# Optimization experiments

Measured on AMD Instinct MI355X. Metric: run time of the kernel, lower is better.

Reference implementation:

```python
import jax, jax.numpy as jnp
import numpy as np

B = 262144
N_DIM = 8
N_SPLIT = 4
DEPTH = 8
WIDTH = 32
ALPHA = 0.6
LOGSCALE_FACTOR = 3.0


def setup_inputs() -> dict:
    key = jax.random.key(0)
    ks = jax.random.split(key, 8)
    n_out = (N_DIM - N_SPLIT) * 2  # 8
    inp = {
        "x": jax.random.normal(ks[0], (B, N_DIM), dtype=jnp.float32),
        "logdet": jnp.zeros((B, 1), dtype=jnp.float32),
        # actnorm params (stacked over depth)
        "b": jnp.zeros((DEPTH, 1, N_DIM), dtype=jnp.float32),
        "logs": jnp.zeros((DEPTH, 1, N_DIM), dtype=jnp.float32),
        # affine coupling params
        "log_gamma": jnp.zeros((DEPTH, 1, N_DIM - N_SPLIT), dtype=jnp.float32),
        "W1": jax.random.normal(ks[1], (DEPTH, N_SPLIT, WIDTH), dtype=jnp.float32) / np.sqrt(N_SPLIT),
        "b1": jnp.zeros((DEPTH, WIDTH), dtype=jnp.float32),
        "W2": jax.random.normal(ks[2], (DEPTH, WIDTH, WIDTH), dtype=jnp.float32) / np.sqrt(WIDTH),
        "b2": jnp.zeros((DEPTH, WIDTH), dtype=jnp.float32),
        "Wf": jax.random.normal(ks[3], (DEPTH, WIDTH, n_out), dtype=jnp.float32) / np.sqrt(WIDTH),
        "bf": jnp.zeros((DEPTH, n_out), dtype=jnp.float32),
    }
    return inp


def _flow_forward(x, logdet, b, logs, log_gamma, W1, b1, W2, b2, Wf, bf):
    z = x
    ld = logdet
    for i in range(DEPTH):
        # ---- actnorm (with data-dependent init, detached as in torch) ----
        m = jnp.mean(z, axis=0, keepdims=True)
        v = jnp.mean(jnp.square(z - m), axis=0, keepdims=True)
        b_init = jax.lax.stop_gradient(-m)
        logs_init = jax.lax.stop_gradient(
            jnp.log(1.0 / (jnp.sqrt(v) + 1e-6)) / LOGSCALE_FACTOR)
        s = jnp.clip(logs[i] + logs_init, -5.0, 5.0)
        z = (z + (b[i] + b_init)) * jnp.exp(s)
        ld = ld + jnp.sum(s)
        # ---- affine coupling ----
        z1 = z[:, :N_SPLIT]
        z2 = z[:, N_SPLIT:]
        h = jax.nn.relu(z1 @ W1[i] + b1[i])
        h = jax.nn.relu(h @ W2[i] + b2[i])
        h = h @ Wf[i] + bf[i]                      # [B, 2*(n_dim-ns)]
        shift = h[:, 0::2]
        scale = ALPHA * jnp.tanh(h[:, 1::2])
        shift = jnp.exp(jnp.clip(log_gamma[i], -5.0, 5.0)) * jnp.tanh(shift)
        z2 = z2 + scale * z2 + shift
        ld = ld + jnp.sum(jnp.log1p(scale), axis=1, keepdims=True)
        z = jnp.concatenate([z1, z2], axis=1)
        # ---- flip ----
        z = z[:, ::-1]
    return z, ld


def reference(x, logdet, b, logs, log_gamma, W1, b1, W2, b2, Wf, bf):
    return _flow_forward(x, logdet, b, logs, log_gamma, W1, b1, W2, b2, Wf, bf)
```

## Files before the change

### kernel.cpp

```cpp
#include <hip/hip_runtime.h>

#define B_ROWS 262144
#define TPB 1024
#define NBLK 256
#define NSLOT 64
#define NGRP 16
#define PADW 32

#define SLOT_DW (16 * NSLOT * PADW)
#define SLOTS_TOTAL_DW (9 * SLOT_DW)

#define GC_OFF   32
#define GF_OFF   (32 + NGRP * PADW)
#define BAR_DWORDS (GF_OFF + NGRP * PADW)

#define ZERO_DWORDS (SLOTS_TOTAL_DW + BAR_DWORDS)

typedef _Float16 f16;
typedef __attribute__((ext_vector_type(2))) __fp16 fp16x2_t;
typedef __attribute__((ext_vector_type(8))) _Float16 f16x8;
typedef __attribute__((ext_vector_type(4))) float f32x4;
typedef __attribute__((ext_vector_type(16))) float f32x16;
typedef __attribute__((ext_vector_type(2))) unsigned u32x2;

__device__ __forceinline__ float fast_tanh(float x) {
    float e = __expf(2.0f * x);
    return 1.0f - 2.0f * __builtin_amdgcn_rcpf(e + 1.0f);
}
__device__ __forceinline__ float pkh(float a, float b) {
    fp16x2_t h = __builtin_amdgcn_cvt_pkrtz(a, b);
    return __builtin_bit_cast(float, h);
}
__device__ __forceinline__ f16x8 mk8(float a, float b, float c, float d) {
    f32x4 v = {a, b, c, d};
    return __builtin_bit_cast(f16x8, v);
}
__device__ __forceinline__ float bcf(unsigned u) { return __builtin_bit_cast(float, u); }
__device__ __forceinline__ u32x2 pls(float a, float b) {
    return __builtin_amdgcn_permlane32_swap(
        __builtin_bit_cast(unsigned, a), __builtin_bit_cast(unsigned, b),
        false, false);
}

__device__ __forceinline__ void gbar(unsigned* bar, unsigned target) {
    __syncthreads();
    if (threadIdx.x == 0) {
        const int g = blockIdx.x >> 4;
        unsigned old = __hip_atomic_fetch_add(bar + GC_OFF + g * PADW, 1u,
                                              __ATOMIC_ACQ_REL,
                                              __HIP_MEMORY_SCOPE_AGENT);
        if (old + 1 == target * (NBLK / NGRP)) {
            unsigned ro = __hip_atomic_fetch_add(bar, 1u, __ATOMIC_ACQ_REL,
                                                 __HIP_MEMORY_SCOPE_AGENT);
            if (ro + 1 == target * NGRP) {
                __threadfence();
                #pragma unroll
                for (int i = 0; i < NGRP; ++i)
                    __hip_atomic_store(bar + GF_OFF + i * PADW, target,
                                       __ATOMIC_RELAXED,
                                       __HIP_MEMORY_SCOPE_AGENT);
            }
        }
        unsigned* gf = bar + GF_OFF + g * PADW;
        while (__hip_atomic_load(gf, __ATOMIC_RELAXED,
                                 __HIP_MEMORY_SCOPE_AGENT) < target)
            __builtin_amdgcn_s_sleep(2);
        (void)__hip_atomic_load(gf, __ATOMIC_ACQUIRE, __HIP_MEMORY_SCOPE_AGENT);
    }
    __syncthreads();
}

#define PKBLK 80
__global__ void __launch_bounds__(256)
pack_weights(const float* __restrict__ W1, const float* __restrict__ W2,
             const float* __restrict__ Wf,
             f16* __restrict__ w1pk, f16* __restrict__ w2pk, f16* __restrict__ wfpk,
             float* __restrict__ zbase)
{
    int i = blockIdx.x * 256 + threadIdx.x;
    if (i < 16384) {
        int which = i >> 13;
        int t  = i & 8191;
        int j  = t & 7;
        int ln = (t >> 3) & 63;
        int kh = (t >> 9) & 1;
        int L  = t >> 10;
        int k  = kh * 16 + ((ln >> 5) << 3) + j;
        if (which == 0) {
            w2pk[t] = (f16)W2[L * 1024 + k * 32 + (ln & 31)];
        } else {
            int row = ln & 31;
            wfpk[t] = (row < 8) ? (f16)Wf[L * 256 + k * 8 + row] : (f16)0.f;
        }
    } else {
        int t  = i - 16384;
        int j  = t & 7;
        int ln = (t >> 3) & 63;
        int L  = t >> 9;
        int k  = ((ln >> 5) << 3) + j;
        w1pk[t] = (k < 4) ? (f16)W1[L * 128 + k * 32 + (ln & 31)] : (f16)0.f;
    }
    float4 zv = {0.f, 0.f, 0.f, 0.f};
    float4* zp = reinterpret_cast<float4*>(zbase);
    const int total4 = ZERO_DWORDS >> 2;
    for (int t4 = i; t4 < total4; t4 += PKBLK * 256)
        zp[t4] = zv;
}

__global__ void __launch_bounds__(TPB, 4)
flow_fused(const float* __restrict__ x,    const float* __restrict__ logdet,
           const float* __restrict__ bvec, const float* __restrict__ logs,
           const float* __restrict__ log_gamma,
           const float* __restrict__ b1,   const float* __restrict__ b2,
           const float* __restrict__ bf,
           const f16* __restrict__ w1pk,   const f16* __restrict__ w2pk,
           const f16* __restrict__ wfpk,
           float* __restrict__ out,        float* slots,
           unsigned* __restrict__ bar)
{
    const int tid  = threadIdx.x;
    const int bid  = blockIdx.x;
    const int lane = tid & 63;
    const int wid  = tid >> 6;
    const bool lo  = lane < 32;
    const int slot = bid & (NSLOT - 1);
    const int br = ((lane & 1) << 3) | ((lane & 2) << 1) | ((lane & 4) >> 1) | ((lane & 8) >> 3);
    const size_t r0 = (size_t)bid * TPB + tid;

    __shared__ float lred[16 * 16];

    float z[8];
    {
        const float4* p0 = reinterpret_cast<const float4*>(x + r0 * 8);
        float4 a = p0[0], c = p0[1];
        z[0]=a.x; z[1]=a.y; z[2]=a.z; z[3]=a.w;
        z[4]=c.x; z[5]=c.y; z[6]=c.z; z[7]=c.w;
    }
    float ldv = logdet[r0];

    {
        float acc[16];
        #pragma unroll
        for (int j = 0; j < 8; ++j) { acc[j] = z[j]; acc[8 + j] = z[j] * z[j]; }
        #pragma unroll
        for (int i = 0; i < 8; ++i) {
            float snd = (lane & 1) ? acc[i] : acc[8 + i];
            float kp  = (lane & 1) ? acc[8 + i] : acc[i];
            acc[i] = kp + __shfl_xor(snd, 1, 64);
        }
        #pragma unroll
        for (int i = 0; i < 4; ++i) {
            float snd = (lane & 2) ? acc[i] : acc[4 + i];
            float kp  = (lane & 2) ? acc[4 + i] : acc[i];
            acc[i] = kp + __shfl_xor(snd, 2, 64);
        }
        #pragma unroll
        for (int i = 0; i < 2; ++i) {
            float snd = (lane & 4) ? acc[i] : acc[2 + i];
            float kp  = (lane & 4) ? acc[2 + i] : acc[i];
            acc[i] = kp + __shfl_xor(snd, 4, 64);
        }
        {
            float snd = (lane & 8) ? acc[0] : acc[1];
            float kp  = (lane & 8) ? acc[1] : acc[0];
            acc[0] = kp + __shfl_xor(snd, 8, 64);
        }
        acc[0] += __shfl_xor(acc[0], 16, 64);
        acc[0] += __shfl_xor(acc[0], 32, 64);
        if (lane < 16) lred[wid * 16 + br] = acc[0];
        __syncthreads();
        if (tid < 16) {
            float s = 0.f;
            #pragma unroll
            for (int w = 0; w < 16; ++w) s += lred[w * 16 + tid];
            __hip_atomic_fetch_add(slots + (size_t)(tid * NSLOT + slot) * PADW, s,
                                   __ATOMIC_RELAXED, __HIP_MEMORY_SCOPE_AGENT);
        }
    }
    gbar(bar, 1);

    const f16x8* w1p = reinterpret_cast<const f16x8*>(w1pk);
    const f16x8* w2p = reinterpret_cast<const f16x8*>(w2pk);
    const f16x8* wfp = reinterpret_cast<const f16x8*>(wfpk);

    #pragma unroll 1
    for (int L = 0; L < 8; ++L) {
        const f16x8 W1A = w1p[L * 64 + lane];
        const f16x8 A0  = w2p[(L * 2 + 0) * 64 + lane];
        const f16x8 A1  = w2p[(L * 2 + 1) * 64 + lane];
        const f16x8 F0  = wfp[(L * 2 + 0) * 64 + lane];
        const f16x8 F1  = wfp[(L * 2 + 1) * 64 + lane];

        float es[8], beta[8], gfac[4], sum_s;
        {
            const float* sl = slots + (size_t)L * SLOT_DW;
            if (wid == 0) {
                float a16[16];
                #pragma unroll
                for (int j = 0; j < 16; ++j)
                    a16[j] = __hip_atomic_load(sl + (size_t)(j * NSLOT + lane) * PADW,
                                               __ATOMIC_RELAXED,
                                               __HIP_MEMORY_SCOPE_AGENT);
                #pragma unroll
                for (int d = 1; d < 64; d <<= 1) {
                    #pragma unroll
                    for (int j = 0; j < 16; ++j) a16[j] += __shfl_xor(a16[j], d, 64);
                }
                const float invB = 1.0f / (float)B_ROWS;
                float lv[21];
                float ss = 0.f;
                #pragma unroll
                for (int j = 0; j < 8; ++j) {
                    float m = a16[j] * invB;
                    float q = a16[8 + j] * invB;
                    float v = q - m * m;
                    v = v < 0.f ? 0.f : v;
                    float li = -(1.0f / 3.0f) * __logf(sqrtf(v) + 1e-6f);
                    float s = logs[L * 8 + j] + li;
                    s = s < -5.f ? -5.f : (s > 5.f ? 5.f : s);
                    lv[j]     = __expf(s);
                    lv[8 + j] = bvec[L * 8 + j] - m;
                    ss += s;
                }
                #pragma unroll
                for (int j = 0; j < 4; ++j) {
                    float lg = log_gamma[L * 4 + j];
                    lg = lg < -5.f ? -5.f : (lg > 5.f ? 5.f : lg);
                    lv[16 + j] = __expf(lg);
                }
                lv[20] = ss;
                if (lane == 0) {
                    #pragma unroll
                    for (int j = 0; j < 21; ++j) lred[j] = lv[j];
                }
            }
            __syncthreads();
            #pragma unroll
            for (int j = 0; j < 8; ++j) { es[j] = lred[j]; beta[j] = lred[8 + j]; }
            #pragma unroll
            for (int j = 0; j < 4; ++j) gfac[j] = lred[16 + j];
            sum_s = lred[20];
            __syncthreads();
        }

        #pragma unroll
        for (int j = 0; j < 8; ++j)
            z[j] = (z[j] + beta[j]) * es[j];

        const float* vb1 = b1 + L * 32;
        const float* vb2 = b2 + L * 32;
        const float* vbf = bf + L * 8;

        float zp0 = pkh(z[0], z[1]);
        float zp1 = pkh(z[2], z[3]);
        u32x2 s0 = pls(zp0, 0.f);
        u32x2 s1 = pls(zp1, 0.f);
        f16x8 Z0 = mk8(bcf(s0[0]), bcf(s1[0]), 0.f, 0.f);
        f16x8 Z1 = mk8(bcf(s0[1]), bcf(s1[1]), 0.f, 0.f);

        f32x16 g0 = {}, g1 = {};
        g0 = __builtin_amdgcn_mfma_f32_32x32x16_f16(W1A, Z0, g0, 0, 0, 0);
        g1 = __builtin_amdgcn_mfma_f32_32x32x16_f16(W1A, Z1, g1, 0, 0, 0);

        float qg0[8], qg1[8];
        {
            float h0[16], h1v[16];
            #pragma unroll
            for (int r = 0; r < 16; ++r) {
                int wlo = (r & 3) + 8 * (r >> 2);
                float bsel = lo ? vb1[wlo] : vb1[wlo + 4];
                float a = g0[r] + bsel; h0[r]  = a > 0.f ? a : 0.f;
                float b = g1[r] + bsel; h1v[r] = b > 0.f ? b : 0.f;
            }
            #pragma unroll
            for (int c = 0; c < 8; ++c) {
                qg0[c] = pkh(h0[2 * c], h0[2 * c + 1]);
                qg1[c] = pkh(h1v[2 * c], h1v[2 * c + 1]);
            }
        }

        u32x2 pA = pls(qg0[0], qg0[2]);
        u32x2 pB = pls(qg0[1], qg0[3]);
        u32x2 pC = pls(qg0[4], qg0[6]);
        u32x2 pD = pls(qg0[5], qg0[7]);
        f16x8 B00 = mk8(bcf(pA[0]), bcf(pB[0]), bcf(pA[1]), bcf(pB[1]));
        f16x8 B01 = mk8(bcf(pC[0]), bcf(pD[0]), bcf(pC[1]), bcf(pD[1]));
        pA = pls(qg1[0], qg1[2]);
        pB = pls(qg1[1], qg1[3]);
        pC = pls(qg1[4], qg1[6]);
        pD = pls(qg1[5], qg1[7]);
        f16x8 B10 = mk8(bcf(pA[0]), bcf(pB[0]), bcf(pA[1]), bcf(pB[1]));
        f16x8 B11 = mk8(bcf(pC[0]), bcf(pD[0]), bcf(pC[1]), bcf(pD[1]));

        f32x16 d0 = {}, d1 = {};
        d0 = __builtin_amdgcn_mfma_f32_32x32x16_f16(A0, B00, d0, 0, 0, 0);
        d0 = __builtin_amdgcn_mfma_f32_32x32x16_f16(A1, B01, d0, 0, 0, 0);
        d1 = __builtin_amdgcn_mfma_f32_32x32x16_f16(A0, B10, d1, 0, 0, 0);
        d1 = __builtin_amdgcn_mfma_f32_32x32x16_f16(A1, B11, d1, 0, 0, 0);

        float P0[8], P1[8];
        {
            float h2g0[16], h2g1[16];
            #pragma unroll
            for (int r = 0; r < 16; ++r) {
                int wlo = (r & 3) + 8 * (r >> 2);
                float bsel = lo ? vb2[wlo] : vb2[wlo + 4];
                float a = d0[r] + bsel; h2g0[r] = a > 0.f ? a : 0.f;
                float b = d1[r] + bsel; h2g1[r] = b > 0.f ? b : 0.f;
            }
            #pragma unroll
            for (int c = 0; c < 8; ++c) {
                P0[c] = pkh(h2g0[2 * c], h2g0[2 * c + 1]);
                P1[c] = pkh(h2g1[2 * c], h2g1[2 * c + 1]);
            }
        }

        u32x2 pE = pls(P0[0], P0[2]);
        u32x2 pF = pls(P0[1], P0[3]);
        u32x2 pG = pls(P0[4], P0[6]);
        u32x2 pH = pls(P0[5], P0[7]);
        f16x8 C00 = mk8(bcf(pE[0]), bcf(pF[0]), bcf(pE[1]), bcf(pF[1]));
        f16x8 C01 = mk8(bcf(pG[0]), bcf(pH[0]), bcf(pG[1]), bcf(pH[1]));
        pE = pls(P1[0], P1[2]);
        pF = pls(P1[1], P1[3]);
        pG = pls(P1[4], P1[6]);
        pH = pls(P1[5], P1[7]);
        f16x8 C10 = mk8(bcf(pE[0]), bcf(pF[0]), bcf(pE[1]), bcf(pF[1]));
        f16x8 C11 = mk8(bcf(pG[0]), bcf(pH[0]), bcf(pG[1]), bcf(pH[1]));

        f32x16 e0 = {}, e1 = {};
        e0 = __builtin_amdgcn_mfma_f32_32x32x16_f16(F0, C00, e0, 0, 0, 0);
        e0 = __builtin_amdgcn_mfma_f32_32x32x16_f16(F1, C01, e0, 0, 0, 0);
        e1 = __builtin_amdgcn_mfma_f32_32x32x16_f16(F0, C10, e1, 0, 0, 0);
        e1 = __builtin_amdgcn_mfma_f32_32x32x16_f16(F1, C11, e1, 0, 0, 0);

        float h3[8];
        #pragma unroll
        for (int r = 0; r < 4; ++r) {
            u32x2 pe = pls(e0[r], e1[r]);
            h3[r]     = bcf(pe[0]) + vbf[r];
            h3[r + 4] = bcf(pe[1]) + vbf[r + 4];
        }

        float nacc[16];
        {
            float ldl = 0.f;
            float nz[8];
            #pragma unroll
            for (int j = 0; j < 4; ++j) {
                float sc = 0.6f * fast_tanh(h3[2 * j + 1]);
                float sh = gfac[j] * fast_tanh(h3[2 * j]);
                float z2 = z[4 + j];
                z2 = z2 + sc * z2 + sh;
                ldl += __logf(1.0f + sc);
                nz[3 - j] = z2;
                nz[7 - j] = z[j];
            }
            ldv += sum_s + ldl;
            #pragma unroll
            for (int j = 0; j < 8; ++j) {
                z[j] = nz[j];
                nacc[j]     = nz[j];
                nacc[8 + j] = nz[j] * nz[j];
            }
        }

        if (L < 7) {
            #pragma unroll
            for (int i = 0; i < 8; ++i) {
                float snd = (lane & 1) ? nacc[i] : nacc[8 + i];
                float kp  = (lane & 1) ? nacc[8 + i] : nacc[i];
                nacc[i] = kp + __shfl_xor(snd, 1, 64);
            }
            #pragma unroll
            for (int i = 0; i < 4; ++i) {
                float snd = (lane & 2) ? nacc[i] : nacc[4 + i];
                float kp  = (lane & 2) ? nacc[4 + i] : nacc[i];
                nacc[i] = kp + __shfl_xor(snd, 2, 64);
            }
            #pragma unroll
            for (int i = 0; i < 2; ++i) {
                float snd = (lane & 4) ? nacc[i] : nacc[2 + i];
                float kp  = (lane & 4) ? nacc[2 + i] : nacc[i];
                nacc[i] = kp + __shfl_xor(snd, 4, 64);
            }
            {
                float snd = (lane & 8) ? nacc[0] : nacc[1];
                float kp  = (lane & 8) ? nacc[1] : nacc[0];
                nacc[0] = kp + __shfl_xor(snd, 8, 64);
            }
            nacc[0] += __shfl_xor(nacc[0], 16, 64);
            nacc[0] += __shfl_xor(nacc[0], 32, 64);
            if (lane < 16) lred[wid * 16 + br] = nacc[0];
            __syncthreads();
            if (tid < 16) {
                float s = 0.f;
                #pragma unroll
                for (int w = 0; w < 16; ++w) s += lred[w * 16 + tid];
                __hip_atomic_fetch_add(slots + (size_t)(L + 1) * SLOT_DW +
                                           (size_t)(tid * NSLOT + slot) * PADW, s,
                                       __ATOMIC_RELAXED, __HIP_MEMORY_SCOPE_AGENT);
            }
            gbar(bar, (unsigned)(L + 2));
        }
    }

    {
        float4* p0 = reinterpret_cast<float4*>(out + r0 * 8);
        float4 a, c;
        a.x=z[0]; a.y=z[1]; a.z=z[2]; a.w=z[3];
        c.x=z[4]; c.y=z[5]; c.z=z[6]; c.w=z[7];
        p0[0] = a; p0[1] = c;
    }
    out[(size_t)B_ROWS * 8 + r0] = ldv;
}

extern "C" void kernel_launch(void* const* d_in, const int* in_sizes, int n_in,
                              void* d_out, int out_size, void* d_ws, size_t ws_size,
                              hipStream_t stream) {
    const float* x      = (const float*)d_in[0];
    const float* logdet = (const float*)d_in[1];
    const float* bvec   = (const float*)d_in[2];
    const float* logs   = (const float*)d_in[3];
    const float* lg     = (const float*)d_in[4];
    const float* W1     = (const float*)d_in[5];
    const float* b1     = (const float*)d_in[6];
    const float* W2     = (const float*)d_in[7];
    const float* b2     = (const float*)d_in[8];
    const float* Wf     = (const float*)d_in[9];
    const float* bf     = (const float*)d_in[10];
    float* out = (float*)d_out;

    f16*      w1pk  = (f16*)d_ws;
    f16*      w2pk  = w1pk + 4096;
    f16*      wfpk  = w2pk + 8192;
    float*    slots = (float*)(wfpk + 8192);
    unsigned* bar   = (unsigned*)(slots + SLOTS_TOTAL_DW);

    pack_weights<<<PKBLK, 256, 0, stream>>>(W1, W2, Wf, w1pk, w2pk, wfpk, slots);

    void* args[] = {&x, &logdet, &bvec, &logs, &lg, &b1, &b2, &bf,
                    &w1pk, &w2pk, &wfpk, &out, &slots, &bar};
    hipLaunchKernel(reinterpret_cast<void*>(&flow_fused),
                    dim3(NBLK), dim3(TPB), args, 0, stream);
}
```

Baseline: 128.3 us.

## Fold actnorm statistics reduction into hierarchical grid barrier

The per-layer column statistics no longer go through scattered float atomics into 64 slots. Each block now plainly stores its 16 partial sums; the last arriving block in each group of 16 sums its group, and the last group finalizer computes the mean, variance, scales and shifts once and publishes them before releasing the barrier. After the barrier, blocks only load 21 precomputed values instead of each running a 16x64 load-and-shuffle reduction. Because the slots no longer need clearing, the large zero-fill in the pack kernel goes away. The cost is a longer serial tail on the barrier's critical path, since single threads do the group and final reductions, and correctness now depends on release/acquire ordering.

```diff
diff --git a/kernel.cpp b/kernel.cpp
--- a/kernel.cpp
+++ b/kernel.cpp
@@ -3,18 +3,18 @@
 #define B_ROWS 262144
 #define TPB 1024
 #define NBLK 256
-#define NSLOT 64
 #define NGRP 16
 #define PADW 32
 
-#define SLOT_DW (16 * NSLOT * PADW)
-#define SLOTS_TOTAL_DW (9 * SLOT_DW)
+#define PART_L_DW (NBLK * PADW)
+#define PART_TOT  (9 * PART_L_DW)
+#define GGRP_L_DW (NGRP * PADW)
+#define GGRP_TOT  (9 * GGRP_L_DW)
+#define STATS_TOT (9 * PADW)
 
 #define GC_OFF   32
 #define GF_OFF   (32 + NGRP * PADW)
 #define BAR_DWORDS (GF_OFF + NGRP * PADW)
-
-#define ZERO_DWORDS (SLOTS_TOTAL_DW + BAR_DWORDS)
 
 typedef _Float16 f16;
 typedef __attribute__((ext_vector_type(2))) __fp16 fp16x2_t;
@@ -42,7 +42,19 @@
         false, false);
 }
 
-__device__ __forceinline__ void gbar(unsigned* bar, unsigned target) {
+#define ACC16(pp) do {                                                      \
+    float4 v0 = (pp)[0], v1 = (pp)[1], v2 = (pp)[2], v3 = (pp)[3];          \
+    s[0]+=v0.x; s[1]+=v0.y; s[2]+=v0.z;  s[3]+=v0.w;                        \
+    s[4]+=v1.x; s[5]+=v1.y; s[6]+=v1.z;  s[7]+=v1.w;                        \
+    s[8]+=v2.x; s[9]+=v2.y; s[10]+=v2.z; s[11]+=v2.w;                       \
+    s[12]+=v3.x; s[13]+=v3.y; s[14]+=v3.z; s[15]+=v3.w;                     \
+} while (0)
+
+__device__ __forceinline__ void gbar_stats(
+    float* part, float* ggrp, float* stats, unsigned* bar,
+    unsigned target, int Lx,
+    const float* logs, const float* bvec, const float* log_gamma)
+{
     __syncthreads();
     if (threadIdx.x == 0) {
         const int g = blockIdx.x >> 4;
@@ -50,14 +62,64 @@
                                               __ATOMIC_ACQ_REL,
                                               __HIP_MEMORY_SCOPE_AGENT);
         if (old + 1 == target * (NBLK / NGRP)) {
+            float s[16];
+            #pragma unroll
+            for (int j = 0; j < 16; ++j) s[j] = 0.f;
+            const float* pb = part + (size_t)Lx * PART_L_DW + (size_t)(g * 16) * PADW;
+            #pragma unroll
+            for (int b = 0; b < 16; ++b) {
+                const float4* pp = reinterpret_cast<const float4*>(pb + b * PADW);
+                ACC16(pp);
+            }
+            float* gg = ggrp + (size_t)Lx * GGRP_L_DW + (size_t)g * PADW;
+            #pragma unroll
+            for (int j = 0; j < 16; ++j)
+                __hip_atomic_store(gg + j, s[j], __ATOMIC_RELAXED,
+                                   __HIP_MEMORY_SCOPE_AGENT);
             unsigned ro = __hip_atomic_fetch_add(bar, 1u, __ATOMIC_ACQ_REL,
                                                  __HIP_MEMORY_SCOPE_AGENT);
             if (ro + 1 == target * NGRP) {
-                __threadfence();
+                float s[16];
+                #pragma unroll
+                for (int j = 0; j < 16; ++j) s[j] = 0.f;
+                const float* gb = ggrp + (size_t)Lx * GGRP_L_DW;
+                #pragma unroll
+                for (int q = 0; q < NGRP; ++q) {
+                    const float4* pp = reinterpret_cast<const float4*>(gb + q * PADW);
+                    ACC16(pp);
+                }
+                const float invB = 1.0f / (float)B_ROWS;
+                float lv[21];
+                float ss = 0.f;
+                #pragma unroll
+                for (int j = 0; j < 8; ++j) {
+                    float m = s[j] * invB;
+                    float q = s[8 + j] * invB;
+                    float v = q - m * m;
+                    v = v < 0.f ? 0.f : v;
+                    float li = -(1.0f / 3.0f) * __logf(sqrtf(v) + 1e-6f);
+                    float sv = logs[Lx * 8 + j] + li;
+                    sv = sv < -5.f ? -5.f : (sv > 5.f ? 5.f : sv);
+                    lv[j]     = __expf(sv);
+                    lv[8 + j] = bvec[Lx * 8 + j] - m;
+                    ss += sv;
+                }
+                #pragma unroll
+                for (int j = 0; j < 4; ++j) {
+                    float lg = log_gamma[Lx * 4 + j];
+                    lg = lg < -5.f ? -5.f : (lg > 5.f ? 5.f : lg);
+                    lv[16 + j] = __expf(lg);
+                }
+                lv[20] = ss;
+                float* st = stats + (size_t)Lx * PADW;
+                #pragma unroll
+                for (int j = 0; j < 21; ++j)
+                    __hip_atomic_store(st + j, lv[j], __ATOMIC_RELAXED,
+                                       __HIP_MEMORY_SCOPE_AGENT);
                 #pragma unroll
                 for (int i = 0; i < NGRP; ++i)
                     __hip_atomic_store(bar + GF_OFF + i * PADW, target,
-                                       __ATOMIC_RELAXED,
+                                       __ATOMIC_RELEASE,
                                        __HIP_MEMORY_SCOPE_AGENT);
             }
         }
@@ -75,7 +137,7 @@
 pack_weights(const float* __restrict__ W1, const float* __restrict__ W2,
              const float* __restrict__ Wf,
              f16* __restrict__ w1pk, f16* __restrict__ w2pk, f16* __restrict__ wfpk,
-             float* __restrict__ zbase)
+             unsigned* __restrict__ bar)
 {
     int i = blockIdx.x * 256 + threadIdx.x;
     if (i < 16384) {
@@ -100,11 +162,7 @@
         int k  = ((ln >> 5) << 3) + j;
         w1pk[t] = (k < 4) ? (f16)W1[L * 128 + k * 32 + (ln & 31)] : (f16)0.f;
     }
-    float4 zv = {0.f, 0.f, 0.f, 0.f};
-    float4* zp = reinterpret_cast<float4*>(zbase);
-    const int total4 = ZERO_DWORDS >> 2;
-    for (int t4 = i; t4 < total4; t4 += PKBLK * 256)
-        zp[t4] = zv;
+    if (i < BAR_DWORDS) bar[i] = 0u;
 }
 
 __global__ void __launch_bounds__(TPB, 4)
@@ -115,7 +173,8 @@
            const float* __restrict__ bf,
            const f16* __restrict__ w1pk,   const f16* __restrict__ w2pk,
            const f16* __restrict__ wfpk,
-           float* __restrict__ out,        float* slots,
+           float* __restrict__ out,
+           float* part, float* ggrp, float* stats,
            unsigned* __restrict__ bar)
 {
     const int tid  = threadIdx.x;
@@ -123,7 +182,6 @@
     const int lane = tid & 63;
     const int wid  = tid >> 6;
     const bool lo  = lane < 32;
-    const int slot = bid & (NSLOT - 1);
     const int br = ((lane & 1) << 3) | ((lane & 2) << 1) | ((lane & 4) >> 1) | ((lane & 8) >> 3);
     const size_t r0 = (size_t)bid * TPB + tid;
 
@@ -173,11 +231,11 @@
             float s = 0.f;
             #pragma unroll
             for (int w = 0; w < 16; ++w) s += lred[w * 16 + tid];
-            __hip_atomic_fetch_add(slots + (size_t)(tid * NSLOT + slot) * PADW, s,
-                                   __ATOMIC_RELAXED, __HIP_MEMORY_SCOPE_AGENT);
-        }
-    }
-    gbar(bar, 1);
+            __hip_atomic_store(part + (size_t)bid * PADW + tid, s,
+                               __ATOMIC_RELAXED, __HIP_MEMORY_SCOPE_AGENT);
+        }
+    }
+    gbar_stats(part, ggrp, stats, bar, 1, 0, logs, bvec, log_gamma);
 
     const f16x8* w1p = reinterpret_cast<const f16x8*>(w1pk);
     const f16x8* w2p = reinterpret_cast<const f16x8*>(w2pk);
@@ -193,47 +251,10 @@
 
         float es[8], beta[8], gfac[4], sum_s;
         {
-            const float* sl = slots + (size_t)L * SLOT_DW;
-            if (wid == 0) {
-                float a16[16];
-                #pragma unroll
-                for (int j = 0; j < 16; ++j)
-                    a16[j] = __hip_atomic_load(sl + (size_t)(j * NSLOT + lane) * PADW,
-                                               __ATOMIC_RELAXED,
+            const float* st = stats + (size_t)L * PADW;
+            if (wid == 0 && lane < 21)
+                lred[lane] = __hip_atomic_load(st + lane, __ATOMIC_RELAXED,
                                                __HIP_MEMORY_SCOPE_AGENT);
-                #pragma unroll
-                for (int d = 1; d < 64; d <<= 1) {
-                    #pragma unroll
-                    for (int j = 0; j < 16; ++j) a16[j] += __shfl_xor(a16[j], d, 64);
-                }
-                const float invB = 1.0f / (float)B_ROWS;
-                float lv[21];
-                float ss = 0.f;
-                #pragma unroll
-                for (int j = 0; j < 8; ++j) {
-                    float m = a16[j] * invB;
-                    float q = a16[8 + j] * invB;
-                    float v = q - m * m;
-                    v = v < 0.f ? 0.f : v;
-                    float li = -(1.0f / 3.0f) * __logf(sqrtf(v) + 1e-6f);
-                    float s = logs[L * 8 + j] + li;
-                    s = s < -5.f ? -5.f : (s > 5.f ? 5.f : s);
-                    lv[j]     = __expf(s);
-                    lv[8 + j] = bvec[L * 8 + j] - m;
-                    ss += s;
-                }
-                #pragma unroll
-                for (int j = 0; j < 4; ++j) {
-                    float lg = log_gamma[L * 4 + j];
-                    lg = lg < -5.f ? -5.f : (lg > 5.f ? 5.f : lg);
-                    lv[16 + j] = __expf(lg);
-                }
-                lv[20] = ss;
-                if (lane == 0) {
-                    #pragma unroll
-                    for (int j = 0; j < 21; ++j) lred[j] = lv[j];
-                }
-            }
             __syncthreads();
             #pragma unroll
             for (int j = 0; j < 8; ++j) { es[j] = lred[j]; beta[j] = lred[8 + j]; }
@@ -397,11 +418,12 @@
                 float s = 0.f;
                 #pragma unroll
                 for (int w = 0; w < 16; ++w) s += lred[w * 16 + tid];
-                __hip_atomic_fetch_add(slots + (size_t)(L + 1) * SLOT_DW +
-                                           (size_t)(tid * NSLOT + slot) * PADW, s,
-                                       __ATOMIC_RELAXED, __HIP_MEMORY_SCOPE_AGENT);
-            }
-            gbar(bar, (unsigned)(L + 2));
+                __hip_atomic_store(part + (size_t)(L + 1) * PART_L_DW +
+                                       (size_t)bid * PADW + tid, s,
+                                   __ATOMIC_RELAXED, __HIP_MEMORY_SCOPE_AGENT);
+            }
+            gbar_stats(part, ggrp, stats, bar, (unsigned)(L + 2), L + 1,
+                       logs, bvec, log_gamma);
         }
     }
 
@@ -434,13 +456,15 @@
     f16*      w1pk  = (f16*)d_ws;
     f16*      w2pk  = w1pk + 4096;
     f16*      wfpk  = w2pk + 8192;
-    float*    slots = (float*)(wfpk + 8192);
-    unsigned* bar   = (unsigned*)(slots + SLOTS_TOTAL_DW);
-
-    pack_weights<<<PKBLK, 256, 0, stream>>>(W1, W2, Wf, w1pk, w2pk, wfpk, slots);
+    float*    part  = (float*)(wfpk + 8192);
+    float*    ggrp  = part + PART_TOT;
+    float*    stats = ggrp + GGRP_TOT;
+    unsigned* bar   = (unsigned*)(stats + STATS_TOT);
+
+    pack_weights<<<PKBLK, 256, 0, stream>>>(W1, W2, Wf, w1pk, w2pk, wfpk, bar);
 
     void* args[] = {&x, &logdet, &bvec, &logs, &lg, &b1, &b2, &bf,
-                    &w1pk, &w2pk, &wfpk, &out, &slots, &bar};
+                    &w1pk, &w2pk, &wfpk, &out, &part, &ggrp, &stats, &bar};
     hipLaunchKernel(reinterpret_cast<void*>(&flow_fused),
                     dim3(NBLK), dim3(TPB), args, 0, stream);
 }
```

Result: slower. 189.7 us (+47.8%).

## Centralize actnorm stats finalization in block 0 inside grid barrier

Applied to the files above, without the earlier changes.

The grid barrier is restructured so that block 0 waits for all groups, reduces the per-slot partial sums, computes the actnorm scale, shift, gamma factors and logdet sum once, and publishes them to a small global stats buffer before releasing the group flags. Other blocks read those 21 values directly instead of each redundantly loading 1024 slot values and doing the reduction and transcendentals themselves. Slot padding is also removed so the partial sums are densely packed, which shrinks the zero-fill in the pack kernel and the load footprint. The trade-off is a serialized finalize step on block 0 inside the critical path of every barrier, plus possible atomic contention on unpadded adjacent slots.

```diff
diff --git a/kernel.cpp b/kernel.cpp
--- a/kernel.cpp
+++ b/kernel.cpp
@@ -3,18 +3,17 @@
 #define B_ROWS 262144
 #define TPB 1024
 #define NBLK 256
-#define NSLOT 64
 #define NGRP 16
 #define PADW 32
 
-#define SLOT_DW (16 * NSLOT * PADW)
-#define SLOTS_TOTAL_DW (9 * SLOT_DW)
+#define SLOT_L_DW (16 * 64)
+#define SLOTS_TOT (9 * SLOT_L_DW)
+#define STATS_L_DW 32
+#define STATS_TOT (9 * STATS_L_DW)
 
 #define GC_OFF   32
 #define GF_OFF   (32 + NGRP * PADW)
 #define BAR_DWORDS (GF_OFF + NGRP * PADW)
-
-#define ZERO_DWORDS (SLOTS_TOTAL_DW + BAR_DWORDS)
 
 typedef _Float16 f16;
 typedef __attribute__((ext_vector_type(2))) __fp16 fp16x2_t;
@@ -42,30 +41,97 @@
         false, false);
 }
 
-__device__ __forceinline__ void gbar(unsigned* bar, unsigned target) {
+__device__ __forceinline__ void gbar_stats(
+    float* slots, float* stats, unsigned* bar, unsigned target, int Lx,
+    const float* logs, const float* bvec, const float* lgam, float* lred)
+{
+    const int tid  = threadIdx.x;
+    const int lane = tid & 63;
+    const int wid  = tid >> 6;
+    const int bid  = blockIdx.x;
     __syncthreads();
-    if (threadIdx.x == 0) {
-        const int g = blockIdx.x >> 4;
-        unsigned old = __hip_atomic_fetch_add(bar + GC_OFF + g * PADW, 1u,
-                                              __ATOMIC_ACQ_REL,
-                                              __HIP_MEMORY_SCOPE_AGENT);
-        if (old + 1 == target * (NBLK / NGRP)) {
-            unsigned ro = __hip_atomic_fetch_add(bar, 1u, __ATOMIC_ACQ_REL,
-                                                 __HIP_MEMORY_SCOPE_AGENT);
-            if (ro + 1 == target * NGRP) {
-                __threadfence();
+    if (wid == 0) {
+        if (lane == 0) {
+            const int g = bid >> 4;
+            unsigned old = __hip_atomic_fetch_add(bar + GC_OFF + g * PADW, 1u,
+                                                  __ATOMIC_ACQ_REL,
+                                                  __HIP_MEMORY_SCOPE_AGENT);
+            if (old + 1 == target * (NBLK / NGRP))
+                __hip_atomic_fetch_add(bar, 1u, __ATOMIC_ACQ_REL,
+                                       __HIP_MEMORY_SCOPE_AGENT);
+        }
+        if (bid == 0) {
+            while (__hip_atomic_load(bar, __ATOMIC_RELAXED,
+                                     __HIP_MEMORY_SCOPE_AGENT) < target * NGRP)
+                __builtin_amdgcn_s_sleep(2);
+            (void)__hip_atomic_load(bar, __ATOMIC_ACQUIRE,
+                                    __HIP_MEMORY_SCOPE_AGENT);
+            const float* sl = slots + (size_t)Lx * SLOT_L_DW;
+            float a16[16];
+            #pragma unroll
+            for (int j = 0; j < 16; ++j)
+                a16[j] = __hip_atomic_load(sl + j * 64 + lane, __ATOMIC_RELAXED,
+                                           __HIP_MEMORY_SCOPE_AGENT);
+            #pragma unroll
+            for (int d = 1; d < 64; d <<= 1) {
                 #pragma unroll
-                for (int i = 0; i < NGRP; ++i)
-                    __hip_atomic_store(bar + GF_OFF + i * PADW, target,
-                                       __ATOMIC_RELAXED,
-                                       __HIP_MEMORY_SCOPE_AGENT);
-            }
-        }
-        unsigned* gf = bar + GF_OFF + g * PADW;
-        while (__hip_atomic_load(gf, __ATOMIC_RELAXED,
-                                 __HIP_MEMORY_SCOPE_AGENT) < target)
-            __builtin_amdgcn_s_sleep(2);
-        (void)__hip_atomic_load(gf, __ATOMIC_ACQUIRE, __HIP_MEMORY_SCOPE_AGENT);
+                for (int j = 0; j < 16; ++j) a16[j] += __shfl_xor(a16[j], d, 64);
+            }
+            const float invB = 1.0f / (float)B_ROWS;
+            float lv0 = 0.f, lv1 = 0.f, sl8 = 0.f, gf = 0.f;
+            if (lane < 8) {
+                float m = a16[lane] * invB;
+                float q = a16[8 + lane] * invB;
+                float v = q - m * m;
+                v = v < 0.f ? 0.f : v;
+                float li = -(1.0f / 3.0f) * __logf(sqrtf(v) + 1e-6f);
+                float s = logs[Lx * 8 + lane] + li;
+                s = s < -5.f ? -5.f : (s > 5.f ? 5.f : s);
+                lv0 = __expf(s);
+                lv1 = bvec[Lx * 8 + lane] - m;
+                sl8 = s;
+            } else if (lane < 12) {
+                float lg = lgam[Lx * 4 + (lane - 8)];
+                lg = lg < -5.f ? -5.f : (lg > 5.f ? 5.f : lg);
+                gf = __expf(lg);
+            }
+            float ss = sl8;
+            ss += __shfl_xor(ss, 1, 64);
+            ss += __shfl_xor(ss, 2, 64);
+            ss += __shfl_xor(ss, 4, 64);
+            float* st = stats + (size_t)Lx * STATS_L_DW;
+            if (lane < 8) {
+                __hip_atomic_store(st + lane, lv0, __ATOMIC_RELAXED,
+                                   __HIP_MEMORY_SCOPE_AGENT);
+                __hip_atomic_store(st + 8 + lane, lv1, __ATOMIC_RELAXED,
+                                   __HIP_MEMORY_SCOPE_AGENT);
+                lred[lane] = lv0; lred[8 + lane] = lv1;
+            } else if (lane < 12) {
+                __hip_atomic_store(st + 8 + lane, gf, __ATOMIC_RELAXED,
+                                   __HIP_MEMORY_SCOPE_AGENT);
+                lred[8 + lane] = gf;
+            }
+            if (lane == 0) {
+                __hip_atomic_store(st + 20, ss, __ATOMIC_RELAXED,
+                                   __HIP_MEMORY_SCOPE_AGENT);
+                lred[20] = ss;
+            }
+            if (lane < NGRP)
+                __hip_atomic_store(bar + GF_OFF + lane * PADW, target,
+                                   __ATOMIC_RELEASE, __HIP_MEMORY_SCOPE_AGENT);
+        } else {
+            const int g = bid >> 4;
+            unsigned* gfp = bar + GF_OFF + g * PADW;
+            while (__hip_atomic_load(gfp, __ATOMIC_RELAXED,
+                                     __HIP_MEMORY_SCOPE_AGENT) < target)
+                __builtin_amdgcn_s_sleep(2);
+            (void)__hip_atomic_load(gfp, __ATOMIC_ACQUIRE,
+                                    __HIP_MEMORY_SCOPE_AGENT);
+            if (lane < 21)
+                lred[lane] = __hip_atomic_load(stats + (size_t)Lx * STATS_L_DW + lane,
+                                               __ATOMIC_RELAXED,
+                                               __HIP_MEMORY_SCOPE_AGENT);
+        }
     }
     __syncthreads();
 }
@@ -75,7 +141,7 @@
 pack_weights(const float* __restrict__ W1, const float* __restrict__ W2,
              const float* __restrict__ Wf,
              f16* __restrict__ w1pk, f16* __restrict__ w2pk, f16* __restrict__ wfpk,
-             float* __restrict__ zbase)
+             float* __restrict__ slots, unsigned* __restrict__ bar)
 {
     int i = blockIdx.x * 256 + threadIdx.x;
     if (i < 16384) {
@@ -100,11 +166,8 @@
         int k  = ((ln >> 5) << 3) + j;
         w1pk[t] = (k < 4) ? (f16)W1[L * 128 + k * 32 + (ln & 31)] : (f16)0.f;
     }
-    float4 zv = {0.f, 0.f, 0.f, 0.f};
-    float4* zp = reinterpret_cast<float4*>(zbase);
-    const int total4 = ZERO_DWORDS >> 2;
-    for (int t4 = i; t4 < total4; t4 += PKBLK * 256)
-        zp[t4] = zv;
+    if (i < SLOTS_TOT) slots[i] = 0.f;
+    if (i < BAR_DWORDS) bar[i] = 0u;
 }
 
 __global__ void __launch_bounds__(TPB, 4)
@@ -115,15 +178,15 @@
            const float* __restrict__ bf,
            const f16* __restrict__ w1pk,   const f16* __restrict__ w2pk,
            const f16* __restrict__ wfpk,
-           float* __restrict__ out,        float* slots,
-           unsigned* __restrict__ bar)
+           float* __restrict__ out,
+           float* slots, float* stats, unsigned* __restrict__ bar)
 {
     const int tid  = threadIdx.x;
     const int bid  = blockIdx.x;
     const int lane = tid & 63;
     const int wid  = tid >> 6;
     const bool lo  = lane < 32;
-    const int slot = bid & (NSLOT - 1);
+    const int slot = bid & 63;
     const int br = ((lane & 1) << 3) | ((lane & 2) << 1) | ((lane & 4) >> 1) | ((lane & 8) >> 3);
     const size_t r0 = (size_t)bid * TPB + tid;
 
@@ -173,11 +236,11 @@
             float s = 0.f;
             #pragma unroll
             for (int w = 0; w < 16; ++w) s += lred[w * 16 + tid];
-            __hip_atomic_fetch_add(slots + (size_t)(tid * NSLOT + slot) * PADW, s,
+            __hip_atomic_fetch_add(slots + tid * 64 + slot, s,
                                    __ATOMIC_RELAXED, __HIP_MEMORY_SCOPE_AGENT);
         }
     }
-    gbar(bar, 1);
+    gbar_stats(slots, stats, bar, 1, 0, logs, bvec, log_gamma, lred);
 
     const f16x8* w1p = reinterpret_cast<const f16x8*>(w1pk);
     const f16x8* w2p = reinterpret_cast<const f16x8*>(w2pk);
@@ -192,56 +255,12 @@
         const f16x8 F1  = wfp[(L * 2 + 1) * 64 + lane];
 
         float es[8], beta[8], gfac[4], sum_s;
-        {
-            const float* sl = slots + (size_t)L * SLOT_DW;
-            if (wid == 0) {
-                float a16[16];
-                #pragma unroll
-                for (int j = 0; j < 16; ++j)
-                    a16[j] = __hip_atomic_load(sl + (size_t)(j * NSLOT + lane) * PADW,
-                                               __ATOMIC_RELAXED,
-                                               __HIP_MEMORY_SCOPE_AGENT);
-                #pragma unroll
-                for (int d = 1; d < 64; d <<= 1) {
-                    #pragma unroll
-                    for (int j = 0; j < 16; ++j) a16[j] += __shfl_xor(a16[j], d, 64);
-                }
-                const float invB = 1.0f / (float)B_ROWS;
-                float lv[21];
-                float ss = 0.f;
-                #pragma unroll
-                for (int j = 0; j < 8; ++j) {
-                    float m = a16[j] * invB;
-                    float q = a16[8 + j] * invB;
-                    float v = q - m * m;
-                    v = v < 0.f ? 0.f : v;
-                    float li = -(1.0f / 3.0f) * __logf(sqrtf(v) + 1e-6f);
-                    float s = logs[L * 8 + j] + li;
-                    s = s < -5.f ? -5.f : (s > 5.f ? 5.f : s);
-                    lv[j]     = __expf(s);
-                    lv[8 + j] = bvec[L * 8 + j] - m;
-                    ss += s;
-                }
-                #pragma unroll
-                for (int j = 0; j < 4; ++j) {
-                    float lg = log_gamma[L * 4 + j];
-                    lg = lg < -5.f ? -5.f : (lg > 5.f ? 5.f : lg);
-                    lv[16 + j] = __expf(lg);
-                }
-                lv[20] = ss;
-                if (lane == 0) {
-                    #pragma unroll
-                    for (int j = 0; j < 21; ++j) lred[j] = lv[j];
-                }
-            }
-            __syncthreads();
-            #pragma unroll
-            for (int j = 0; j < 8; ++j) { es[j] = lred[j]; beta[j] = lred[8 + j]; }
-            #pragma unroll
-            for (int j = 0; j < 4; ++j) gfac[j] = lred[16 + j];
-            sum_s = lred[20];
-            __syncthreads();
-        }
+        #pragma unroll
+        for (int j = 0; j < 8; ++j) { es[j] = lred[j]; beta[j] = lred[8 + j]; }
+        #pragma unroll
+        for (int j = 0; j < 4; ++j) gfac[j] = lred[16 + j];
+        sum_s = lred[20];
+        __syncthreads();
 
         #pragma unroll
         for (int j = 0; j < 8; ++j)
@@ -397,11 +416,12 @@
                 float s = 0.f;
                 #pragma unroll
                 for (int w = 0; w < 16; ++w) s += lred[w * 16 + tid];
-                __hip_atomic_fetch_add(slots + (size_t)(L + 1) * SLOT_DW +
-                                           (size_t)(tid * NSLOT + slot) * PADW, s,
+                __hip_atomic_fetch_add(slots + (size_t)(L + 1) * SLOT_L_DW +
+                                           tid * 64 + slot, s,
                                        __ATOMIC_RELAXED, __HIP_MEMORY_SCOPE_AGENT);
             }
-            gbar(bar, (unsigned)(L + 2));
+            gbar_stats(slots, stats, bar, (unsigned)(L + 2), L + 1,
+                       logs, bvec, log_gamma, lred);
         }
     }
 
@@ -435,12 +455,14 @@
     f16*      w2pk  = w1pk + 4096;
     f16*      wfpk  = w2pk + 8192;
     float*    slots = (float*)(wfpk + 8192);
-    unsigned* bar   = (unsigned*)(slots + SLOTS_TOTAL_DW);
-
-    pack_weights<<<PKBLK, 256, 0, stream>>>(W1, W2, Wf, w1pk, w2pk, wfpk, slots);
+    float*    stats = slots + SLOTS_TOT;
+    unsigned* bar   = (unsigned*)(stats + STATS_TOT);
+
+    pack_weights<<<PKBLK, 256, 0, stream>>>(W1, W2, Wf, w1pk, w2pk, wfpk,
+                                            slots, bar);
 
     void* args[] = {&x, &logdet, &bvec, &logs, &lg, &b1, &b2, &bf,
-                    &w1pk, &w2pk, &wfpk, &out, &slots, &bar};
+                    &w1pk, &w2pk, &wfpk, &out, &slots, &stats, &bar};
     hipLaunchKernel(reinterpret_cast<void*>(&flow_fused),
                     dim3(NBLK), dim3(TPB), args, 0, stream);
 }
```

Result: faster. 112.2 us (-12.6%).
